# Optimization experiments

Measured on AMD Instinct MI355X. Metric: run time of the kernel, lower is better.

Reference implementation:

```python
import jax, jax.numpy as jnp
import numpy as np

GRID = 18          # grid_dim
NTYPES = 6         # n_atom_types
SIGMA_P = 0.6      # sigma * bins_per_angstrom
B = 256            # number of environments (batch)
ATOMS_PER_ENV = 100
N = B * ATOMS_PER_ENV
EPS = 1e-5
SLOPE = 0.01       # LeakyReLU default negative slope


def _grid_points():
    # lin_spacing(): centers of 18 unit bins, -8.5 .. 8.5
    ls = np.linspace(-GRID / 2 + 0.5, GRID / 2 - 0.5, GRID)
    xx, yy, zz = np.meshgrid(ls, ls, ls, indexing='ij')
    return jnp.asarray(np.stack([xx, yy, zz], -1).reshape(-1, 3), jnp.float32)  # [G,3]


def _leaky(x):
    return jnp.where(x >= 0, x, SLOPE * x)


def _bn(x, g, b):
    # batch-norm with batch statistics (torch training-mode math), channel axis 1
    axes = tuple(i for i in range(x.ndim) if i != 1)
    m = x.mean(axes, keepdims=True)
    v = x.var(axes, keepdims=True)
    shp = [1] * x.ndim
    shp[1] = -1
    return (x - m) / jnp.sqrt(v + EPS) * g.reshape(shp) + b.reshape(shp)


def _conv3d(x, w, b, pad):
    y = jax.lax.conv_general_dilated(
        x, w, window_strides=(1, 1, 1), padding=[(pad, pad)] * 3,
        dimension_numbers=('NCDHW', 'OIDHW', 'NCDHW'))
    return y + b[None, :, None, None, None]


def _maxpool2(x):
    return jax.lax.reduce_window(x, -jnp.inf, jax.lax.max,
                                 (1, 1, 2, 2, 2), (1, 1, 2, 2, 2), 'VALID')


def _gaussian_blurring(pos, batch_ids, types):
    grid = _grid_points()                                  # [G,3], G=5832
    # squared distances via ||a-b||^2 = ||a||^2 + ||b||^2 - 2 a.b  -> avoids [G,N,3]
    d2 = (jnp.sum(grid * grid, -1)[:, None]
          + jnp.sum(pos * pos, -1)[None, :]
          - 2.0 * grid @ pos.T)                            # [G,N]
    dens = jnp.exp(-d2 / (2.0 * SIGMA_P ** 2))
    dens = dens / jnp.sum(dens, axis=0, keepdims=True)     # normalize per atom
    seg = batch_ids * NTYPES + types                       # [N]
    fields = jax.ops.segment_sum(dens.T, seg, num_segments=B * NTYPES)  # [B*6,G]
    return fields.reshape(B, NTYPES, GRID, GRID, GRID)


def setup_inputs() -> dict:
    key = jax.random.key(0)
    ks = jax.random.split(key, 16)
    pos = jax.random.uniform(ks[0], (N, 3), jnp.float32, -8.5, 8.5)
    batch_ids = jnp.repeat(jnp.arange(B, dtype=jnp.int32), ATOMS_PER_ENV)
    types = (jnp.arange(N, dtype=jnp.int32) % NTYPES)  # every env has every type
    s = 0.05
    return {
        'pos': pos,
        'c1w': jax.random.normal(ks[1], (16, 6, 3, 3, 3), jnp.float32) * s,
        'c1b': jax.random.normal(ks[2], (16,), jnp.float32) * s,
        'bn1g': jnp.ones((16,), jnp.float32), 'bn1b': jnp.zeros((16,), jnp.float32),
        'c2w': jax.random.normal(ks[3], (32, 16, 3, 3, 3), jnp.float32) * s,
        'c2b': jax.random.normal(ks[4], (32,), jnp.float32) * s,
        'bn2g': jnp.ones((32,), jnp.float32), 'bn2b': jnp.zeros((32,), jnp.float32),
        'c3w': jax.random.normal(ks[5], (64, 32, 3, 3, 3), jnp.float32) * s,
        'c3b': jax.random.normal(ks[6], (64,), jnp.float32) * s,
        'bn3g': jnp.ones((64,), jnp.float32), 'bn3b': jnp.zeros((64,), jnp.float32),
        'd1w': jax.random.normal(ks[7], (128, 64), jnp.float32) * s,
        'd1b': jax.random.normal(ks[8], (128,), jnp.float32) * s,
        'bn4g': jnp.ones((128,), jnp.float32), 'bn4b': jnp.zeros((128,), jnp.float32),
        'd2w': jax.random.normal(ks[9], (100, 128), jnp.float32) * s,
        'd2b': jax.random.normal(ks[10], (100,), jnp.float32) * s,
        'd3w': jax.random.normal(ks[11], (20, 100), jnp.float32) * s,
        'd3b': jax.random.normal(ks[12], (20,), jnp.float32) * s,
        'batch_ids': batch_ids,
        'types': types,
    }


def reference(pos, c1w, c1b, bn1g, bn1b, c2w, c2b, bn2g, bn2b, c3w, c3b, bn3g, bn3b,
              d1w, d1b, bn4g, bn4b, d2w, d2b, d3w, d3b, batch_ids, types):
    x = _gaussian_blurring(pos, batch_ids, types)            # [B,6,18,18,18]
    x = _leaky(_bn(_maxpool2(_conv3d(x, c1w, c1b, 1)), bn1g, bn1b))  # [B,16,9,9,9]
    x = _leaky(_bn(_maxpool2(_conv3d(x, c2w, c2b, 0)), bn2g, bn2b))  # [B,32,3,3,3]
    x = _leaky(_bn(_maxpool2(_conv3d(x, c3w, c3b, 1)), bn3g, bn3b))  # [B,64,1,1,1]
    x = x.reshape(x.shape[0], -1)                            # [B,64]
    x = _leaky(_bn(x @ d1w.T + d1b, bn4g, bn4b))             # [B,128]
    x = x @ d2w.T + d2b                                      # [B,100]
    x = _leaky(x)
    x = x @ d3w.T + d3b                                      # [B,20]
    return x
```

## Files before the change

kernel.cpp:

```cpp
#include <hip/hip_runtime.h>


#define G2 324
#define G3 5832
#define NT 6
#define BATCH 256
#define APE 100
#define EPS 1e-5f

typedef unsigned short u16;
typedef unsigned int u32;
typedef _Float16 h2 __attribute__((ext_vector_type(2)));

__device__ __forceinline__ float leaky(float x) { return x >= 0.0f ? x : 0.01f * x; }
__device__ __forceinline__ u32 pkh(float a, float b) {
    h2 v; v[0] = (_Float16)a; v[1] = (_Float16)b;
    return __builtin_bit_cast(u32, v);
}
__device__ __forceinline__ float fdot2u(u32 a, u32 b, float c) {
#if __has_builtin(__builtin_amdgcn_fdot2)
    return __builtin_amdgcn_fdot2(__builtin_bit_cast(h2, a),
                                  __builtin_bit_cast(h2, b), c, false);
#else
    h2 x = __builtin_bit_cast(h2, a), y = __builtin_bit_cast(h2, b);
    return c + (float)x[0] * (float)y[0] + (float)x[1] * (float)y[1];
#endif
}

__global__ __launch_bounds__(512) void k_splat(const float* __restrict__ pos,
        const int* __restrict__ types, u32* __restrict__ fields) {
    __shared__ float ew[APE * 54];
    __shared__ float ssum[APE * 3];
    __shared__ int list[APE];
    __shared__ int base[NT + 1];
    __shared__ int cnt[NT], cur[NT];
    const int b = blockIdx.x, tid = threadIdx.x;

    if (tid < NT) { cnt[tid] = 0; cur[tid] = 0; }
    __syncthreads();
    if (tid < APE) atomicAdd(&cnt[types[b * APE + tid]], 1);
    if (tid < 300) {
        const int la = tid / 3, ax = tid % 3;
        const float p = pos[(b * APE + la) * 3 + ax];
        float s = 0.0f;
        #pragma unroll
        for (int g = 0; g < 18; ++g) {
            const float d = (float)g - 8.5f - p;
            const float e = __expf(d * d * (-1.0f / 0.72f));
            ew[la * 54 + ax * 18 + g] = e;
            s += e;
        }
        ssum[tid] = s;
    }
    __syncthreads();
    if (tid == 0) {
        int s = 0;
        #pragma unroll
        for (int t = 0; t < NT; ++t) { base[t] = s; s += cnt[t]; }
        base[NT] = s;
    }
    if (tid < APE) {
        const float inv = 1.0f / (ssum[tid * 3] * ssum[tid * 3 + 1] * ssum[tid * 3 + 2]);
        #pragma unroll
        for (int g = 0; g < 18; ++g) ew[tid * 54 + g] *= inv;
    }
    __syncthreads();
    if (tid < APE) {
        const int t = types[b * APE + tid];
        const int j = atomicAdd(&cur[t], 1);
        list[base[t] + j] = tid;
    }
    __syncthreads();

    for (int it = tid; it < NT * 324; it += 512) {
        const int t = it / 324, r = it - t * 324;
        const int i = r / 18, j = r % 18;
        float acc[18];
        #pragma unroll
        for (int k = 0; k < 18; ++k) acc[k] = 0.0f;
        const int e1 = base[t + 1];
        for (int u = base[t]; u < e1; ++u) {
            const int a = list[u];
            const float exy = ew[a * 54 + i] * ew[a * 54 + 18 + j];
            const float* ez = &ew[a * 54 + 36];
            #pragma unroll
            for (int k = 0; k < 18; ++k) acc[k] += exy * ez[k];
        }
        u32* dst = &fields[((size_t)b * NT + t) * 2916 + (size_t)r * 9];
        #pragma unroll
        for (int q = 0; q < 9; ++q) dst[q] = pkh(acc[2 * q], acc[2 * q + 1]);
    }
}

template <int ZG>
__device__ __forceinline__ void conv1_pass(int c2, int Xl, int Yv, int b, int Xg,
        const u32* fldH, const u32* wpk, float* s_sum, float* s_ssq,
        const float* __restrict__ bias, float* __restrict__ a1) {
    float acc[2][2][2][6];
    #pragma unroll
    for (int c = 0; c < 2; ++c)
        #pragma unroll
        for (int o = 0; o < 2; ++o)
            #pragma unroll
            for (int p = 0; p < 2; ++p)
                #pragma unroll
                for (int z = 0; z < 6; ++z) acc[c][o][p][z] = 0.0f;

    for (int ic = 0; ic < 6; ++ic) {
        u32 A0[9], A1[9], Be0[9], Be1[9];
        #pragma unroll
        for (int d2 = 0; d2 < 9; ++d2) {
            const int wb = ((ic * 9 + d2) * 8 + c2) * 3;
            A0[d2] = wpk[wb]; A1[d2] = wpk[wb + 1];
            const u32 w2 = wpk[wb + 2];
            Be0[d2] = w2 & 0xFFFFu; Be1[d2] = w2 >> 16;
        }
        #pragma unroll
        for (int lj = 0; lj < 4; ++lj) {
            const int iy = 2 * Yv + lj - 1;
            const bool yok = (iy >= 0 && iy < 18);
            #pragma unroll
            for (int li = 0; li < 4; ++li) {
                const int ixl = 2 * Xl + li;
                u32 V[5], Sh[4];
                if (yok) {
                    const u32* rp = &fldH[((ic * 8 + ixl) * 18 + iy) * 10];
                    if (ZG == 0) {
                        V[0] = 0u;
                        #pragma unroll
                        for (int q = 0; q < 4; ++q) V[q + 1] = rp[q];
                    } else {
                        #pragma unroll
                        for (int q = 0; q < 5; ++q) V[q] = rp[3 * ZG - 1 + q];
                    }
                } else {
                    #pragma unroll
                    for (int q = 0; q < 5; ++q) V[q] = 0u;
                }
                #pragma unroll
                for (int q = 0; q < 4; ++q)
                    Sh[q] = __builtin_amdgcn_alignbit(V[q + 1], V[q], 16);
                #pragma unroll
                for (int o = 0; o < 2; ++o) {
                    const int dx = li - o;
                    if (dx < 0 || dx > 2) continue;
                    #pragma unroll
                    for (int p = 0; p < 2; ++p) {
                        const int dy = lj - p;
                        if (dy < 0 || dy > 2) continue;
                        const int d2 = dx * 3 + dy;
                        #pragma unroll
                        for (int ozl = 0; ozl < 6; ++ozl) {
                            if (ozl & 1) {
                                const int vi = (ozl - 1) / 2 + 1;
                                acc[0][o][p][ozl] = fdot2u(A0[d2], V[vi],
                                    fdot2u(Be0[d2], V[vi + 1], acc[0][o][p][ozl]));
                                acc[1][o][p][ozl] = fdot2u(A1[d2], V[vi],
                                    fdot2u(Be1[d2], V[vi + 1], acc[1][o][p][ozl]));
                            } else {
                                const int si = ozl / 2;
                                acc[0][o][p][ozl] = fdot2u(A0[d2], Sh[si],
                                    fdot2u(Be0[d2], Sh[si + 1], acc[0][o][p][ozl]));
                                acc[1][o][p][ozl] = fdot2u(A1[d2], Sh[si],
                                    fdot2u(Be1[d2], Sh[si + 1], acc[1][o][p][ozl]));
                            }
                        }
                    }
                }
            }
        }
    }
    const float bb0 = bias[2 * c2], bb1 = bias[2 * c2 + 1];
    float s0 = 0.0f, q0 = 0.0f, s1 = 0.0f, q1 = 0.0f;
    #pragma unroll
    for (int Zp = 0; Zp < 3; ++Zp) {
        float m0 = acc[0][0][0][2 * Zp], m1 = acc[1][0][0][2 * Zp];
        #pragma unroll
        for (int o = 0; o < 2; ++o)
            #pragma unroll
            for (int p = 0; p < 2; ++p) {
                m0 = fmaxf(m0, fmaxf(acc[0][o][p][2 * Zp], acc[0][o][p][2 * Zp + 1]));
                m1 = fmaxf(m1, fmaxf(acc[1][o][p][2 * Zp], acc[1][o][p][2 * Zp + 1]));
            }
        float2 vv; vv.x = m0 + bb0; vv.y = m1 + bb1;
        s0 += vv.x; q0 += vv.x * vv.x; s1 += vv.y; q1 += vv.y * vv.y;
        const int spg = (3 * Xg + Xl) * 81 + Yv * 9 + 3 * ZG + Zp;
        *(float2*)&a1[((size_t)b * 729 + spg) * 16 + 2 * c2] = vv;
    }
    atomicAdd(&s_sum[2 * c2], s0);     atomicAdd(&s_ssq[2 * c2], q0);
    atomicAdd(&s_sum[2 * c2 + 1], s1); atomicAdd(&s_ssq[2 * c2 + 1], q1);
}

__global__ __launch_bounds__(256, 3) void k_conv1(const u32* __restrict__ fields,
        const float* __restrict__ w, const float* __restrict__ bias,
        float* __restrict__ a1, float* __restrict__ stO) {
    __shared__ u32 fldH[48 * 18 * 10];
    __shared__ u32 wpk[432 * 3];
    __shared__ float s_sum[16], s_ssq[16];
    const int bx = blockIdx.x, b = bx / 3, Xg = bx % 3, tid = threadIdx.x;

    for (int i = tid; i < 432; i += 256) {
        const int c2 = i & 7, t = i >> 3, d2 = t % 9, ic = t / 9;
        const int w0 = (2 * c2) * 162 + ic * 27 + d2 * 3;
        const int w1 = w0 + 162;
        wpk[i * 3]     = pkh(w[w0], w[w0 + 1]);
        wpk[i * 3 + 1] = pkh(w[w1], w[w1 + 1]);
        wpk[i * 3 + 2] = pkh(w[w0 + 2], w[w1 + 2]);
    }
    if (tid < 16) { s_sum[tid] = 0.0f; s_ssq[tid] = 0.0f; }
    for (int i = tid; i < 8640; i += 256) {
        const int p = i % 10, t = i / 10;
        const int iy = t % 18, a = t / 18;
        const int ix = 6 * Xg - 1 + (a & 7);
        u32 v = 0;
        if (p < 9 && ix >= 0 && ix < 18)
            v = fields[((size_t)(b * 6 + (a >> 3)) * 324 + ix * 18 + iy) * 9 + p];
        fldH[t * 10 + p] = v;
    }
    __syncthreads();

    const int c2 = tid & 7, sp = tid >> 3;
    if (tid < 216) {
        const int Xl = sp / 9, Yv = sp % 9;
        conv1_pass<0>(c2, Xl, Yv, b, Xg, fldH, wpk, s_sum, s_ssq, bias, a1);
        conv1_pass<1>(c2, Xl, Yv, b, Xg, fldH, wpk, s_sum, s_ssq, bias, a1);
        conv1_pass<2>(c2, Xl, Yv, b, Xg, fldH, wpk, s_sum, s_ssq, bias, a1);
    }
    __syncthreads();
    if (tid < 16) { atomicAdd(&stO[tid], s_sum[tid]); atomicAdd(&stO[16 + tid], s_ssq[tid]); }
}

__global__ __launch_bounds__(576) void k_conv2(const float* __restrict__ a1,
        const float* __restrict__ w, const float* __restrict__ bias,
        const float* __restrict__ bng, const float* __restrict__ bnb,
        const float* __restrict__ stI, float* __restrict__ a2,
        float* __restrict__ stO) {
    __shared__ float xin[16 * 729];
    __shared__ float ws2[13824];
    __shared__ float sc[16], sh[16];
    __shared__ float s_sum[32], s_ssq[32];
    const int b = blockIdx.x, tid = threadIdx.x;
    if (tid < 16) {
        const float cnt = 256.0f * 729.0f;
        float m = stI[tid] / cnt;
        float v = stI[16 + tid] / cnt - m * m;
        float s = bng[tid] * rsqrtf(fmaxf(v, 0.0f) + EPS);
        sc[tid] = s; sh[tid] = bnb[tid] - m * s;
    }
    if (tid < 32) { s_sum[tid] = 0.0f; s_ssq[tid] = 0.0f; }
    __syncthreads();
    const float* src = a1 + (size_t)b * 729 * 16;
    for (int i = tid; i < 16 * 729; i += 576) {
        const int spb = i >> 4, c = i & 15;
        xin[c * 729 + spb] = leaky(src[i] * sc[c] + sh[c]);
    }
    for (int i = tid; i < 13824; i += 576) ws2[i] = w[i];
    __syncthreads();
    {
        const int oyi = tid & 1, oxi = (tid >> 1) & 1, rest = tid >> 2;
        const int Y = rest % 3, X = (rest / 3) % 3, c2 = rest / 9;
        const int ox = 2 * X + oxi, oy = 2 * Y + oyi;
        const int c0 = 2 * c2, c1 = c0 + 1;
        float acc0[6], acc1[6];
        #pragma unroll
        for (int z = 0; z < 6; ++z) { acc0[z] = 0.0f; acc1[z] = 0.0f; }
        for (int ic = 0; ic < 16; ++ic) {
            #pragma unroll
            for (int dx = 0; dx < 3; ++dx) {
                const int ix = ox + dx;
                #pragma unroll
                for (int dy = 0; dy < 3; ++dy) {
                    const int iy = oy + dy;
                    const float* rp = &xin[ic * 729 + ix * 81 + iy * 9];
                    float row[9];
                    #pragma unroll
                    for (int z = 0; z < 9; ++z) row[z] = rp[z];
                    const int wb0 = (c0 * 16 + ic) * 27 + dx * 9 + dy * 3;
                    const int wb1 = (c1 * 16 + ic) * 27 + dx * 9 + dy * 3;
                    #pragma unroll
                    for (int dz = 0; dz < 3; ++dz) {
                        const float w0 = ws2[wb0 + dz];
                        const float w1v = ws2[wb1 + dz];
                        #pragma unroll
                        for (int z = 0; z < 6; ++z) {
                            acc0[z] += w0 * row[z + dz];
                            acc1[z] += w1v * row[z + dz];
                        }
                    }
                }
            }
        }
        float pl[2][3];
        #pragma unroll
        for (int Z = 0; Z < 3; ++Z) {
            float v0 = fmaxf(acc0[2 * Z], acc0[2 * Z + 1]);
            float v1 = fmaxf(acc1[2 * Z], acc1[2 * Z + 1]);
            v0 = fmaxf(v0, __shfl_xor(v0, 1)); v0 = fmaxf(v0, __shfl_xor(v0, 2));
            v1 = fmaxf(v1, __shfl_xor(v1, 1)); v1 = fmaxf(v1, __shfl_xor(v1, 2));
            pl[0][Z] = v0; pl[1][Z] = v1;
        }
        if ((tid & 3) == 0) {
            #pragma unroll
            for (int hh = 0; hh < 2; ++hh) {
                const int c = c0 + hh;
                const float bb = bias[c];
                float s0 = 0.0f, q0 = 0.0f;
                #pragma unroll
                for (int Z = 0; Z < 3; ++Z) {
                    const float v = pl[hh][Z] + bb;
                    a2[((size_t)b * 32 + c) * 27 + X * 9 + Y * 3 + Z] = v;
                    s0 += v; q0 += v * v;
                }
                atomicAdd(&s_sum[c], s0); atomicAdd(&s_ssq[c], q0);
            }
        }
    }
    __syncthreads();
    if (tid < 32) { atomicAdd(&stO[tid], s_sum[tid]); atomicAdd(&stO[32 + tid], s_ssq[tid]); }
}

__global__ __launch_bounds__(256) void k_conv3(const float* __restrict__ a2,
        const float* __restrict__ w, const float* __restrict__ bias,
        const float* __restrict__ bng, const float* __restrict__ bnb,
        const float* __restrict__ stI, float* __restrict__ a3,
        float* __restrict__ stO) {
    __shared__ float x[864];
    __shared__ float pacc[256 * 8];
    __shared__ float sc[32], sh[32];
    const int b = blockIdx.x, tid = threadIdx.x;
    if (tid < 32) {
        const float cnt = 256.0f * 27.0f;
        float m = stI[tid] / cnt;
        float v = stI[32 + tid] / cnt - m * m;
        float s = bng[tid] * rsqrtf(fmaxf(v, 0.0f) + EPS);
        sc[tid] = s; sh[tid] = bnb[tid] - m * s;
    }
    __syncthreads();
    for (int i = tid; i < 864; i += 256) {
        int c = i / 27;
        x[i] = leaky(a2[(size_t)b * 864 + i] * sc[c] + sh[c]);
    }
    __syncthreads();
    const int c = tid & 63, q = tid >> 6;
    float acc[8];
    #pragma unroll
    for (int p = 0; p < 8; ++p) acc[p] = 0.0f;
    for (int ic = q * 8; ic < q * 8 + 8; ++ic) {
        const float* wr = w + ((size_t)c * 32 + ic) * 27;
        #pragma unroll
        for (int d = 0; d < 27; ++d) {
            const int dx = d / 9, dy = (d / 3) % 3, dz = d % 3;
            const float wv = wr[d];
            #pragma unroll
            for (int p = 0; p < 8; ++p) {
                const int px = p >> 2, py = (p >> 1) & 1, pz = p & 1;
                const int ix = px + dx - 1, iy = py + dy - 1, iz = pz + dz - 1;
                if (ix >= 0 && iy >= 0 && iz >= 0)
                    acc[p] += wv * x[ic * 27 + ix * 9 + iy * 3 + iz];
            }
        }
    }
    #pragma unroll
    for (int p = 0; p < 8; ++p) pacc[tid * 8 + p] = acc[p];
    __syncthreads();
    if (q == 0) {
        float m = -1e30f;
        #pragma unroll
        for (int p = 0; p < 8; ++p) {
            float v = pacc[c * 8 + p] + pacc[(64 + c) * 8 + p]
                    + pacc[(128 + c) * 8 + p] + pacc[(192 + c) * 8 + p];
            m = fmaxf(m, v);
        }
        float v = m + bias[c];
        a3[(size_t)b * 64 + c] = v;
        atomicAdd(&stO[c], v); atomicAdd(&stO[64 + c], v * v);
    }
}

__global__ __launch_bounds__(128) void k_dense1(const float* __restrict__ a3,
        const float* __restrict__ bng, const float* __restrict__ bnb,
        const float* __restrict__ stI,
        const float* __restrict__ w1, const float* __restrict__ b1,
        float* __restrict__ h1, float* __restrict__ stO) {
    __shared__ float x[64];
    const int b = blockIdx.x, tid = threadIdx.x;
    if (tid < 64) {
        float m = stI[tid] / 256.0f;
        float v = stI[64 + tid] / 256.0f - m * m;
        float s = bng[tid] * rsqrtf(fmaxf(v, 0.0f) + EPS);
        x[tid] = leaky(a3[(size_t)b * 64 + tid] * s + (bnb[tid] - m * s));
    }
    __syncthreads();
    const float* wr = w1 + tid * 64;
    float acc = b1[tid];
    #pragma unroll
    for (int i = 0; i < 64; ++i) acc += x[i] * wr[i];
    h1[(size_t)b * 128 + tid] = acc;
    atomicAdd(&stO[tid], acc); atomicAdd(&stO[128 + tid], acc * acc);
}

__global__ __launch_bounds__(128) void k_dense2(const float* __restrict__ h1,
        const float* __restrict__ bng, const float* __restrict__ bnb,
        const float* __restrict__ stI,
        const float* __restrict__ w2, const float* __restrict__ bias2,
        const float* __restrict__ w3, const float* __restrict__ bias3,
        float* __restrict__ out) {
    __shared__ float x[128];
    __shared__ float y[100];
    const int b = blockIdx.x, tid = threadIdx.x;
    {
        float m = stI[tid] / 256.0f;
        float v = stI[128 + tid] / 256.0f - m * m;
        float s = bng[tid] * rsqrtf(fmaxf(v, 0.0f) + EPS);
        x[tid] = leaky(h1[(size_t)b * 128 + tid] * s + (bnb[tid] - m * s));
    }
    __syncthreads();
    if (tid < 100) {
        const float* wr = w2 + tid * 128;
        float acc = bias2[tid];
        #pragma unroll
        for (int i = 0; i < 128; ++i) acc += x[i] * wr[i];
        y[tid] = leaky(acc);
    }
    __syncthreads();
    if (tid < 20) {
        const float* wr = w3 + tid * 100;
        float acc = bias3[tid];
        #pragma unroll
        for (int i = 0; i < 100; ++i) acc += y[i] * wr[i];
        out[(size_t)b * 20 + tid] = acc;
    }
}

extern "C" void kernel_launch(void* const* d_in, const int* in_sizes, int n_in,
                              void* d_out, int out_size, void* d_ws, size_t ws_size,
                              hipStream_t stream) {
    (void)in_sizes; (void)n_in; (void)out_size; (void)ws_size;
    const float* pos  = (const float*)d_in[0];
    const float* c1w  = (const float*)d_in[1];
    const float* c1b  = (const float*)d_in[2];
    const float* bn1g = (const float*)d_in[3];
    const float* bn1b = (const float*)d_in[4];
    const float* c2w  = (const float*)d_in[5];
    const float* c2b  = (const float*)d_in[6];
    const float* bn2g = (const float*)d_in[7];
    const float* bn2b = (const float*)d_in[8];
    const float* c3w  = (const float*)d_in[9];
    const float* c3b  = (const float*)d_in[10];
    const float* bn3g = (const float*)d_in[11];
    const float* bn3b = (const float*)d_in[12];
    const float* d1w  = (const float*)d_in[13];
    const float* d1b  = (const float*)d_in[14];
    const float* bn4g = (const float*)d_in[15];
    const float* bn4b = (const float*)d_in[16];
    const float* d2w  = (const float*)d_in[17];
    const float* d2b  = (const float*)d_in[18];
    const float* d3w  = (const float*)d_in[19];
    const float* d3b  = (const float*)d_in[20];
    const int* types  = (const int*)d_in[22];

    float* ws = (float*)d_ws;
    float* st = ws;
    float* a3 = ws + 512;
    float* h1 = a3 + 16384;
    float* a2 = h1 + 32768;
    float* a1 = a2 + 221184;
    u32* fields = (u32*)(a1 + 2985984);

    hipMemsetAsync(st, 0, 480 * sizeof(float), stream);
    k_splat <<<BATCH, 512, 0, stream>>>(pos, types, fields);
    k_conv1 <<<3 * BATCH, 256, 0, stream>>>(fields, c1w, c1b, a1, st);
    k_conv2 <<<BATCH, 576, 0, stream>>>(a1, c2w, c2b, bn1g, bn1b, st, a2, st + 32);
    k_conv3 <<<BATCH, 256, 0, stream>>>(a2, c3w, c3b, bn2g, bn2b, st + 32, a3, st + 96);
    k_dense1<<<BATCH, 128, 0, stream>>>(a3, bn3g, bn3b, st + 96, d1w, d1b, h1, st + 224);
    k_dense2<<<BATCH, 128, 0, stream>>>(h1, bn4g, bn4b, st + 224, d2w, d2b, d3w, d3b,
                                        (float*)d_out);
}
```

Measured before the change: 236.8 us.

## Split conv2 output channels across two blocks; use scalar FMA for conv1 tail taps

conv2 now launches two blocks per batch element, each computing 16 of the 32 output channels with half the weights in shared memory. This halves per-block LDS use and doubles the grid, aiming for better occupancy and more parallelism, at the cost of loading and normalizing each input twice. Separately, conv1 replaces the fdot2 calls whose second half-lane was zero with fp32 fmaf on pre-converted halves. This removes the wasted packed operation but adds conversion instructions and register pressure.

```diff
diff --git a/kernel.cpp b/kernel.cpp
--- a/kernel.cpp
+++ b/kernel.cpp
@@ -107,13 +107,14 @@
                 for (int z = 0; z < 6; ++z) acc[c][o][p][z] = 0.0f;
 
     for (int ic = 0; ic < 6; ++ic) {
-        u32 A0[9], A1[9], Be0[9], Be1[9];
+        u32 A0[9], A1[9];
+        float Bf0[9], Bf1[9];
         #pragma unroll
         for (int d2 = 0; d2 < 9; ++d2) {
             const int wb = ((ic * 9 + d2) * 8 + c2) * 3;
             A0[d2] = wpk[wb]; A1[d2] = wpk[wb + 1];
-            const u32 w2 = wpk[wb + 2];
-            Be0[d2] = w2 & 0xFFFFu; Be1[d2] = w2 >> 16;
+            const h2 w2 = __builtin_bit_cast(h2, wpk[wb + 2]);
+            Bf0[d2] = (float)w2[0]; Bf1[d2] = (float)w2[1];
         }
         #pragma unroll
         for (int lj = 0; lj < 4; ++lj) {
@@ -140,6 +141,14 @@
                 #pragma unroll
                 for (int q = 0; q < 4; ++q)
                     Sh[q] = __builtin_amdgcn_alignbit(V[q + 1], V[q], 16);
+                float vlo[3], vhi[3];
+                #pragma unroll
+                for (int q = 0; q < 3; ++q) {
+                    const h2 hv = __builtin_bit_cast(h2, V[q + 2]);
+                    vlo[q] = (float)hv[0];
+                    const h2 hw = __builtin_bit_cast(h2, V[q + 1]);
+                    vhi[q] = (float)hw[1];
+                }
                 #pragma unroll
                 for (int o = 0; o < 2; ++o) {
                     const int dx = li - o;
@@ -152,17 +161,17 @@
                         #pragma unroll
                         for (int ozl = 0; ozl < 6; ++ozl) {
                             if (ozl & 1) {
-                                const int vi = (ozl - 1) / 2 + 1;
+                                const int vi = (ozl + 1) >> 1;
                                 acc[0][o][p][ozl] = fdot2u(A0[d2], V[vi],
-                                    fdot2u(Be0[d2], V[vi + 1], acc[0][o][p][ozl]));
+                                    fmaf(Bf0[d2], vlo[vi - 1], acc[0][o][p][ozl]));
                                 acc[1][o][p][ozl] = fdot2u(A1[d2], V[vi],
-                                    fdot2u(Be1[d2], V[vi + 1], acc[1][o][p][ozl]));
+                                    fmaf(Bf1[d2], vlo[vi - 1], acc[1][o][p][ozl]));
                             } else {
-                                const int si = ozl / 2;
+                                const int si = ozl >> 1;
                                 acc[0][o][p][ozl] = fdot2u(A0[d2], Sh[si],
-                                    fdot2u(Be0[d2], Sh[si + 1], acc[0][o][p][ozl]));
+                                    fmaf(Bf0[d2], vhi[si], acc[0][o][p][ozl]));
                                 acc[1][o][p][ozl] = fdot2u(A1[d2], Sh[si],
-                                    fdot2u(Be1[d2], Sh[si + 1], acc[1][o][p][ozl]));
+                                    fmaf(Bf1[d2], vhi[si], acc[1][o][p][ozl]));
                             }
                         }
                     }
@@ -230,37 +239,37 @@
     if (tid < 16) { atomicAdd(&stO[tid], s_sum[tid]); atomicAdd(&stO[16 + tid], s_ssq[tid]); }
 }
 
-__global__ __launch_bounds__(576) void k_conv2(const float* __restrict__ a1,
+__global__ __launch_bounds__(320) void k_conv2(const float* __restrict__ a1,
         const float* __restrict__ w, const float* __restrict__ bias,
         const float* __restrict__ bng, const float* __restrict__ bnb,
         const float* __restrict__ stI, float* __restrict__ a2,
         float* __restrict__ stO) {
     __shared__ float xin[16 * 729];
-    __shared__ float ws2[13824];
+    __shared__ float ws2[6912];
     __shared__ float sc[16], sh[16];
-    __shared__ float s_sum[32], s_ssq[32];
-    const int b = blockIdx.x, tid = threadIdx.x;
+    __shared__ float s_sum[16], s_ssq[16];
+    const int bx = blockIdx.x, b = bx >> 1, half = bx & 1, tid = threadIdx.x;
     if (tid < 16) {
         const float cnt = 256.0f * 729.0f;
         float m = stI[tid] / cnt;
         float v = stI[16 + tid] / cnt - m * m;
         float s = bng[tid] * rsqrtf(fmaxf(v, 0.0f) + EPS);
         sc[tid] = s; sh[tid] = bnb[tid] - m * s;
-    }
-    if (tid < 32) { s_sum[tid] = 0.0f; s_ssq[tid] = 0.0f; }
+        s_sum[tid] = 0.0f; s_ssq[tid] = 0.0f;
+    }
     __syncthreads();
     const float* src = a1 + (size_t)b * 729 * 16;
-    for (int i = tid; i < 16 * 729; i += 576) {
+    for (int i = tid; i < 16 * 729; i += 320) {
         const int spb = i >> 4, c = i & 15;
         xin[c * 729 + spb] = leaky(src[i] * sc[c] + sh[c]);
     }
-    for (int i = tid; i < 13824; i += 576) ws2[i] = w[i];
-    __syncthreads();
-    {
+    for (int i = tid; i < 6912; i += 320) ws2[i] = w[half * 6912 + i];
+    __syncthreads();
+    if (tid < 288) {
         const int oyi = tid & 1, oxi = (tid >> 1) & 1, rest = tid >> 2;
         const int Y = rest % 3, X = (rest / 3) % 3, c2 = rest / 9;
         const int ox = 2 * X + oxi, oy = 2 * Y + oyi;
-        const int c0 = 2 * c2, c1 = c0 + 1;
+        const int cl0 = 2 * c2, cl1 = cl0 + 1;
         float acc0[6], acc1[6];
         #pragma unroll
         for (int z = 0; z < 6; ++z) { acc0[z] = 0.0f; acc1[z] = 0.0f; }
@@ -275,8 +284,8 @@
                     float row[9];
                     #pragma unroll
                     for (int z = 0; z < 9; ++z) row[z] = rp[z];
-                    const int wb0 = (c0 * 16 + ic) * 27 + dx * 9 + dy * 3;
-                    const int wb1 = (c1 * 16 + ic) * 27 + dx * 9 + dy * 3;
+                    const int wb0 = (cl0 * 16 + ic) * 27 + dx * 9 + dy * 3;
+                    const int wb1 = (cl1 * 16 + ic) * 27 + dx * 9 + dy * 3;
                     #pragma unroll
                     for (int dz = 0; dz < 3; ++dz) {
                         const float w0 = ws2[wb0 + dz];
@@ -302,7 +311,7 @@
         if ((tid & 3) == 0) {
             #pragma unroll
             for (int hh = 0; hh < 2; ++hh) {
-                const int c = c0 + hh;
+                const int cl = cl0 + hh, c = half * 16 + cl;
                 const float bb = bias[c];
                 float s0 = 0.0f, q0 = 0.0f;
                 #pragma unroll
@@ -311,12 +320,15 @@
                     a2[((size_t)b * 32 + c) * 27 + X * 9 + Y * 3 + Z] = v;
                     s0 += v; q0 += v * v;
                 }
-                atomicAdd(&s_sum[c], s0); atomicAdd(&s_ssq[c], q0);
+                atomicAdd(&s_sum[cl], s0); atomicAdd(&s_ssq[cl], q0);
             }
         }
     }
     __syncthreads();
-    if (tid < 32) { atomicAdd(&stO[tid], s_sum[tid]); atomicAdd(&stO[32 + tid], s_ssq[tid]); }
+    if (tid < 16) {
+        const int c = half * 16 + tid;
+        atomicAdd(&stO[c], s_sum[tid]); atomicAdd(&stO[32 + c], s_ssq[tid]);
+    }
 }
 
 __global__ __launch_bounds__(256) void k_conv3(const float* __restrict__ a2,
@@ -470,7 +482,7 @@
     hipMemsetAsync(st, 0, 480 * sizeof(float), stream);
     k_splat <<<BATCH, 512, 0, stream>>>(pos, types, fields);
     k_conv1 <<<3 * BATCH, 256, 0, stream>>>(fields, c1w, c1b, a1, st);
-    k_conv2 <<<BATCH, 576, 0, stream>>>(a1, c2w, c2b, bn1g, bn1b, st, a2, st + 32);
+    k_conv2 <<<2 * BATCH, 320, 0, stream>>>(a1, c2w, c2b, bn1g, bn1b, st, a2, st + 32);
     k_conv3 <<<BATCH, 256, 0, stream>>>(a2, c3w, c3b, bn2g, bn2b, st + 32, a3, st + 96);
     k_dense1<<<BATCH, 128, 0, stream>>>(a3, bn3g, bn3b, st + 96, d1w, d1b, h1, st + 224);
     k_dense2<<<BATCH, 128, 0, stream>>>(h1, bn4g, bn4b, st + 224, d2w, d2b, d3w, d3b,
```

Result: slower. 247.4 us (+4.5%).
